# Kernel tuning notes

Measured on AMD Instinct MI355X. Metric: run time of the kernel, lower is better.

Reference implementation:

```python
import jax, jax.numpy as jnp
import numpy as np

HIDDEN = 768
INNER = 512
EPS = 1e-5


def setup_inputs() -> dict:
    key = jax.random.key(0)
    ks = jax.random.split(key, 6)
    B, S = 8, 4096
    x = jax.random.normal(ks[0], (B, S, HIDDEN), dtype=jnp.float32)
    W1 = jax.random.normal(ks[1], (INNER, HIDDEN), dtype=jnp.float32) * 0.02
    b1 = jnp.zeros((INNER,), dtype=jnp.float32)
    W2 = jax.random.normal(ks[2], (HIDDEN, INNER), dtype=jnp.float32) * 0.02
    b2 = jnp.zeros((HIDDEN,), dtype=jnp.float32)
    # output_proj: nn.Linear(hidden, hidden)
    bound = 1.0 / np.sqrt(HIDDEN)
    Wo = jax.random.uniform(ks[3], (HIDDEN, HIDDEN), minval=-bound, maxval=bound, dtype=jnp.float32)
    bo = jax.random.uniform(ks[4], (HIDDEN,), minval=-bound, maxval=bound, dtype=jnp.float32)
    # LayerNorm affine params
    gamma = jnp.ones((HIDDEN,), dtype=jnp.float32)
    beta = jnp.zeros((HIDDEN,), dtype=jnp.float32)
    return {"x": x, "W1": W1, "b1": b1, "W2": W2, "b2": b2,
            "Wo": Wo, "bo": bo, "gamma": gamma, "beta": beta}


def reference(x, W1, b1, W2, b2, Wo, bo, gamma, beta):
    # NOTE: the torch module's inner 'TTT update' loop never actually modifies
    # W1/b1/W2/b2 (loss computed, no step applied), so the math per token is
    # independent and fully vectorizable across (batch, seq).
    h = jax.nn.relu(jnp.einsum('bsd,id->bsi', x, W1) + b1)       # [B,S,INNER]
    pred = jnp.einsum('bsi,di->bsd', h, W2) + b2                 # [B,S,HIDDEN]
    out = jnp.einsum('bsd,ed->bse', pred, Wo) + bo               # output_proj
    # LayerNorm over last dim
    mu = jnp.mean(out, axis=-1, keepdims=True)
    var = jnp.mean(jnp.square(out - mu), axis=-1, keepdims=True)
    out = (out - mu) * jax.lax.rsqrt(var + EPS) * gamma + beta
    return out
```

## Files before the change

kernel.cpp:

```cpp
#include <hip/hip_runtime.h>
#include <hip/hip_bf16.h>


#define HIDDEN 768
#define INNER  512

typedef __bf16 bf16_t;
typedef bf16_t bf16x8 __attribute__((ext_vector_type(8)));
typedef bf16_t bf16x4 __attribute__((ext_vector_type(4)));
typedef float  f32x4  __attribute__((ext_vector_type(4)));

__device__ __forceinline__ void async16(const void* g, void* lds) {
  __builtin_amdgcn_global_load_lds(
      (const __attribute__((address_space(1))) unsigned int*)g,
      (__attribute__((address_space(3))) unsigned int*)lds, 16, 0, 0);
}

__global__ __launch_bounds__(256)
void prep(const float* __restrict__ x, const float* __restrict__ W1,
          const float* __restrict__ W2, const float* __restrict__ Wo,
          bf16_t* __restrict__ xb, bf16_t* __restrict__ W1b,
          bf16_t* __restrict__ W2t, bf16_t* __restrict__ Wob, int xb_blocks) {
  __shared__ float T[64][65];
  const int b = blockIdx.x, t = threadIdx.x;

  const float4* src; bf16x4* dst; int base;
  if (b < xb_blocks)            { src = (const float4*)x;  dst = (bf16x4*)xb;  base = b * 4096; }
  else if (b < xb_blocks + 24)  { src = (const float4*)W1; dst = (bf16x4*)W1b; base = (b - xb_blocks) * 4096; }
  else if (b < xb_blocks + 60)  { src = (const float4*)Wo; dst = (bf16x4*)Wob; base = (b - xb_blocks - 24) * 4096; }
  else {
    const int tile = b - xb_blocks - 60;
    const int d0 = (tile >> 3) << 6;
    const int i0 = (tile & 7) << 6;
#pragma unroll
    for (int j = 0; j < 4; ++j) {
      const int idx = j * 256 + t;
      const int r = idx >> 4, c4 = idx & 15;
      float4 v = *(const float4*)(W2 + (size_t)(d0 + r) * INNER + i0 + c4 * 4);
      T[r][c4 * 4 + 0] = v.x; T[r][c4 * 4 + 1] = v.y;
      T[r][c4 * 4 + 2] = v.z; T[r][c4 * 4 + 3] = v.w;
    }
    __syncthreads();
    const int i = t & 63, h4 = t >> 6;
    bf16x8 o0, o1;
#pragma unroll
    for (int c = 0; c < 8; ++c) { o0[c] = (bf16_t)T[h4 * 16 + c][i]; o1[c] = (bf16_t)T[h4 * 16 + 8 + c][i]; }
    bf16_t* orow = W2t + (size_t)(i0 + i) * HIDDEN + d0 + h4 * 16;
    *(bf16x8*)orow = o0;
    *(bf16x8*)(orow + 8) = o1;
    return;
  }
#pragma unroll
  for (int i = 0; i < 16; ++i) {
    float4 v = src[base + i * 256 + t];
    bf16x4 o;
    o[0] = (bf16_t)v.x; o[1] = (bf16_t)v.y; o[2] = (bf16_t)v.z; o[3] = (bf16_t)v.w;
    dst[base + i * 256 + t] = o;
  }
}

__global__ __launch_bounds__(256)
void beq_k(const float* __restrict__ Wo, const float* __restrict__ b2,
           const float* __restrict__ bo, float* __restrict__ beq) {
  const int e = blockIdx.x * 4 + (threadIdx.x >> 6);
  const int l = threadIdx.x & 63;
  float s = 0.f;
#pragma unroll
  for (int j = 0; j < 12; ++j) s += Wo[(size_t)e * HIDDEN + j * 64 + l] * b2[j * 64 + l];
#pragma unroll
  for (int off = 1; off < 64; off <<= 1) s += __shfl_xor(s, off, 64);
  if (l == 0) beq[e] = s + bo[e];
}

template <int N_, int K_, int MODE>
__global__ __launch_bounds__(256, 2)
void gemm_bt(const bf16_t* __restrict__ A, const bf16_t* __restrict__ Bt,
             const float* __restrict__ bias, bf16_t* __restrict__ Cout) {
  constexpr int NT = N_ / 128;
  constexpr int T  = K_ / 64;
  __shared__ __align__(16) bf16_t As[2][128 * 64];
  __shared__ __align__(16) bf16_t Bs[2][128 * 64];

  const int per = gridDim.x >> 3;
  const int nb  = (blockIdx.x & 7) * per + (blockIdx.x >> 3);
  const int m0 = (nb / NT) * 128;
  const int n0 = (nb % NT) * 128;

  const int tid = threadIdx.x;
  const int w = tid >> 6, l = tid & 63;
  const int wr = w >> 1, wc = w & 1;
  const int fr = l & 15, fq = l >> 4;

#define STAGE(dst, src, r0, k0)                                               \
  _Pragma("unroll") for (int i = 0; i < 4; ++i) {                             \
    const int G = i * 256 + tid, row = G >> 3, g = G & 7;                     \
    async16((src) + (size_t)((r0) + row) * K_ + (k0) + ((g ^ (row & 7)) << 3),\
            (char*)(dst) + (size_t)(i * 256 + w * 64) * 16);                  \
  }

  STAGE(As[0], A, m0, 0); STAGE(Bs[0], Bt, n0, 0);
  __syncthreads();

  f32x4 acc[4][4] = {};
#pragma unroll
  for (int t = 0; t < T; ++t) {
    const int cur = t & 1;
    if (t < T - 1) {
      STAGE(As[cur ^ 1], A, m0, (t + 1) * 64);
      STAGE(Bs[cur ^ 1], Bt, n0, (t + 1) * 64);
    }
#pragma unroll
    for (int kk = 0; kk < 2; ++kk) {
      bf16x8 ax[4], bx[4];
#pragma unroll
      for (int m = 0; m < 4; ++m) {
        const int row = wr * 64 + m * 16 + fr;
        const int slot = (kk * 4 + fq) ^ (row & 7);
        ax[m] = *(const bf16x8*)((const char*)As[cur] + row * 128 + slot * 16);
      }
#pragma unroll
      for (int n = 0; n < 4; ++n) {
        const int row = wc * 64 + n * 16 + fr;
        const int slot = (kk * 4 + fq) ^ (row & 7);
        bx[n] = *(const bf16x8*)((const char*)Bs[cur] + row * 128 + slot * 16);
      }
#pragma unroll
      for (int m = 0; m < 4; ++m)
#pragma unroll
        for (int n = 0; n < 4; ++n)
          acc[m][n] = __builtin_amdgcn_mfma_f32_16x16x32_bf16(ax[m], bx[n], acc[m][n], 0, 0, 0);
    }
    __syncthreads();
  }
#undef STAGE

  const int orow0 = m0 + wr * 64 + fq * 4;
  const int ocol0 = n0 + wc * 64 + fr;
#pragma unroll
  for (int n = 0; n < 4; ++n) {
    const int col = ocol0 + n * 16;
    const float bv = (MODE == 2) ? 0.f : bias[col];
#pragma unroll
    for (int m = 0; m < 4; ++m)
#pragma unroll
      for (int j = 0; j < 4; ++j) {
        float v = acc[m][n][j] + bv;
        if (MODE == 0) v = fmaxf(v, 0.f);
        Cout[(size_t)(orow0 + m * 16 + j) * N_ + col] = (bf16_t)v;
      }
  }
}

__global__ __launch_bounds__(256)
void ln_bf16(const bf16_t* __restrict__ raw, const float* __restrict__ gamma,
             const float* __restrict__ beta, float* __restrict__ out) {
  const int r = blockIdx.x * 4 + (threadIdx.x >> 6);
  const int l = threadIdx.x & 63;
  const bf16_t* rp = raw + (size_t)r * HIDDEN;
  float v[12];
  float s = 0.f, q = 0.f;
#pragma unroll
  for (int c = 0; c < 3; ++c) {
    bf16x4 b4 = *(const bf16x4*)(rp + c * 256 + l * 4);
#pragma unroll
    for (int j = 0; j < 4; ++j) {
      const float f = (float)b4[j];
      v[c * 4 + j] = f; s += f; q += f * f;
    }
  }
#pragma unroll
  for (int off = 1; off < 64; off <<= 1) {
    s += __shfl_xor(s, off, 64);
    q += __shfl_xor(q, off, 64);
  }
  const float mu  = s * (1.0f / HIDDEN);
  const float var = fmaxf(q * (1.0f / HIDDEN) - mu * mu, 0.f);
  const float inv = rsqrtf(var + 1e-5f);
  float* op = out + (size_t)r * HIDDEN;
#pragma unroll
  for (int c = 0; c < 3; ++c) {
    float4 g = ((const float4*)gamma)[c * 64 + l];
    float4 b = ((const float4*)beta)[c * 64 + l];
    float4 o;
    o.x = (v[c * 4 + 0] - mu) * inv * g.x + b.x;
    o.y = (v[c * 4 + 1] - mu) * inv * g.y + b.y;
    o.z = (v[c * 4 + 2] - mu) * inv * g.z + b.z;
    o.w = (v[c * 4 + 3] - mu) * inv * g.w + b.w;
    ((float4*)op)[c * 64 + l] = o;
  }
}

extern "C" void kernel_launch(void* const* d_in, const int* in_sizes, int n_in,
                              void* d_out, int out_size, void* d_ws, size_t ws_size,
                              hipStream_t stream) {
  const float* x     = (const float*)d_in[0];
  const float* W1    = (const float*)d_in[1];
  const float* b1    = (const float*)d_in[2];
  const float* W2    = (const float*)d_in[3];
  const float* b2    = (const float*)d_in[4];
  const float* Wo    = (const float*)d_in[5];
  const float* bo    = (const float*)d_in[6];
  const float* gamma = (const float*)d_in[7];
  const float* beta  = (const float*)d_in[8];

  const int M = in_sizes[0] / HIDDEN;

  char* ws = (char*)d_ws;
  bf16_t* xb   = (bf16_t*)ws;
  bf16_t* raw  = xb;
  bf16_t* h    = (bf16_t*)(ws + (size_t)M * HIDDEN * 2);
  bf16_t* W1b  = (bf16_t*)(ws + (size_t)M * HIDDEN * 2 + (size_t)M * INNER * 2);
  bf16_t* W2t  = W1b + INNER * HIDDEN;
  bf16_t* Wob  = W2t + INNER * HIDDEN;
  bf16_t* Weq  = Wob + HIDDEN * HIDDEN;
  float*  beq  = (float*)(Weq + HIDDEN * INNER);

  const int xb_blocks = (M * HIDDEN / 4) / 4096;

  prep<<<xb_blocks + 60 + 96, 256, 0, stream>>>(x, W1, W2, Wo, xb, W1b, W2t, Wob, xb_blocks);
  beq_k<<<HIDDEN / 4, 256, 0, stream>>>(Wo, b2, bo, beq);

  gemm_bt<INNER, HIDDEN, 2><<<(HIDDEN / 128) * (INNER / 128), 256, 0, stream>>>(Wob, W2t, nullptr, Weq);
  gemm_bt<INNER, HIDDEN, 0><<<(M / 128) * (INNER / 128), 256, 0, stream>>>(xb, W1b, b1, h);
  gemm_bt<HIDDEN, INNER, 1><<<(M / 128) * (HIDDEN / 128), 256, 0, stream>>>(h, Weq, beq, raw);
  ln_bf16<<<M / 4, 256, 0, stream>>>(raw, gamma, beta, (float*)d_out);
}
```

Measured before the change: 140.5 us.

## Use 128x256 tiles with triple-buffered async loads for the large GEMMs

The two large GEMMs move to a new kernel with 512-thread blocks and 128x256 output tiles. It uses a three-stage LDS ring filled by async global-to-LDS loads, explicit vmcnt waits so one stage stays in flight, and raised wave priority around the MFMA section. The aim is to hide global load latency and raise MFMA utilization through more B reuse per tile. The cost is a large LDS footprint (144 KB), which allows only one block per CU and halves the number of blocks in the grid. The small weight-folding GEMM is split into its own non-templated kernel with no bias.

```diff
diff --git a/kernel.cpp b/kernel.cpp
--- a/kernel.cpp
+++ b/kernel.cpp
@@ -72,12 +72,10 @@
   if (l == 0) beq[e] = s + bo[e];
 }
 
-template <int N_, int K_, int MODE>
 __global__ __launch_bounds__(256, 2)
-void gemm_bt(const bf16_t* __restrict__ A, const bf16_t* __restrict__ Bt,
-             const float* __restrict__ bias, bf16_t* __restrict__ Cout) {
-  constexpr int NT = N_ / 128;
-  constexpr int T  = K_ / 64;
+void gemm_small(const bf16_t* __restrict__ A, const bf16_t* __restrict__ Bt,
+                bf16_t* __restrict__ Cout) {
+  constexpr int N_ = INNER, K_ = HIDDEN, NT = N_ / 128, T = K_ / 64;
   __shared__ __align__(16) bf16_t As[2][128 * 64];
   __shared__ __align__(16) bf16_t Bs[2][128 * 64];
 
@@ -91,14 +89,14 @@
   const int wr = w >> 1, wc = w & 1;
   const int fr = l & 15, fq = l >> 4;
 
-#define STAGE(dst, src, r0, k0)                                               \
+#define STAGE2(dst, src, r0, k0)                                              \
   _Pragma("unroll") for (int i = 0; i < 4; ++i) {                             \
     const int G = i * 256 + tid, row = G >> 3, g = G & 7;                     \
     async16((src) + (size_t)((r0) + row) * K_ + (k0) + ((g ^ (row & 7)) << 3),\
             (char*)(dst) + (size_t)(i * 256 + w * 64) * 16);                  \
   }
 
-  STAGE(As[0], A, m0, 0); STAGE(Bs[0], Bt, n0, 0);
+  STAGE2(As[0], A, m0, 0); STAGE2(Bs[0], Bt, n0, 0);
   __syncthreads();
 
   f32x4 acc[4][4] = {};
@@ -106,8 +104,8 @@
   for (int t = 0; t < T; ++t) {
     const int cur = t & 1;
     if (t < T - 1) {
-      STAGE(As[cur ^ 1], A, m0, (t + 1) * 64);
-      STAGE(Bs[cur ^ 1], Bt, n0, (t + 1) * 64);
+      STAGE2(As[cur ^ 1], A, m0, (t + 1) * 64);
+      STAGE2(Bs[cur ^ 1], Bt, n0, (t + 1) * 64);
     }
 #pragma unroll
     for (int kk = 0; kk < 2; ++kk) {
@@ -132,14 +130,103 @@
     }
     __syncthreads();
   }
-#undef STAGE
+#undef STAGE2
 
   const int orow0 = m0 + wr * 64 + fq * 4;
   const int ocol0 = n0 + wc * 64 + fr;
 #pragma unroll
+  for (int n = 0; n < 4; ++n)
+#pragma unroll
+    for (int m = 0; m < 4; ++m)
+#pragma unroll
+      for (int j = 0; j < 4; ++j)
+        Cout[(size_t)(orow0 + m * 16 + j) * N_ + ocol0 + n * 16] = (bf16_t)acc[m][n][j];
+}
+
+template <int N_, int K_, int MODE>
+__global__ __launch_bounds__(512, 1)
+void gemm_p3(const bf16_t* __restrict__ A, const bf16_t* __restrict__ Bt,
+             const float* __restrict__ bias, bf16_t* __restrict__ Cout) {
+  constexpr int NT = N_ / 256;
+  constexpr int T  = K_ / 64;
+  __shared__ __align__(16) bf16_t As[3][128 * 64];
+  __shared__ __align__(16) bf16_t Bs[3][256 * 64];
+
+  const int per = gridDim.x >> 3;
+  const int nb  = (blockIdx.x & 7) * per + (blockIdx.x >> 3);
+  const int m0 = (nb / NT) * 128;
+  const int n0 = (nb % NT) * 256;
+
+  const int tid = threadIdx.x;
+  const int w = tid >> 6, l = tid & 63;
+  const int wm = w >> 2, wn = w & 3;
+  const int fr = l & 15, fq = l >> 4;
+
+#define STAGE_A(buf, k0)                                                      \
+  _Pragma("unroll") for (int i = 0; i < 2; ++i) {                             \
+    const int G = i * 512 + tid, row = G >> 3, g = G & 7;                     \
+    async16(A + (size_t)(m0 + row) * K_ + (k0) + ((g ^ (row & 7)) << 3),      \
+            (char*)As[buf] + (size_t)(i * 512 + w * 64) * 16);                \
+  }
+#define STAGE_B(buf, k0)                                                      \
+  _Pragma("unroll") for (int i = 0; i < 4; ++i) {                             \
+    const int G = i * 512 + tid, row = G >> 3, g = G & 7;                     \
+    async16(Bt + (size_t)(n0 + row) * K_ + (k0) + ((g ^ (row & 7)) << 3),     \
+            (char*)Bs[buf] + (size_t)(i * 512 + w * 64) * 16);                \
+  }
+
+  STAGE_A(0, 0);  STAGE_B(0, 0);
+  STAGE_A(1, 64); STAGE_B(1, 64);
+  asm volatile("s_waitcnt vmcnt(6)" ::: "memory");
+  __builtin_amdgcn_s_barrier();
+
+  f32x4 acc[4][4] = {};
+#pragma unroll
+  for (int t = 0; t < T; ++t) {
+    const int cur = t % 3;
+    if (t + 2 < T) {
+      const int nx = (t + 2) % 3;
+      STAGE_A(nx, (t + 2) * 64);
+      STAGE_B(nx, (t + 2) * 64);
+    }
+    __builtin_amdgcn_s_setprio(1);
+#pragma unroll
+    for (int kk = 0; kk < 2; ++kk) {
+      bf16x8 ax[4], bx[4];
+#pragma unroll
+      for (int m = 0; m < 4; ++m) {
+        const int row = wm * 64 + m * 16 + fr;
+        const int slot = (kk * 4 + fq) ^ (row & 7);
+        ax[m] = *(const bf16x8*)((const char*)As[cur] + row * 128 + slot * 16);
+      }
+#pragma unroll
+      for (int n = 0; n < 4; ++n) {
+        const int row = wn * 64 + n * 16 + fr;
+        const int slot = (kk * 4 + fq) ^ (row & 7);
+        bx[n] = *(const bf16x8*)((const char*)Bs[cur] + row * 128 + slot * 16);
+      }
+#pragma unroll
+      for (int m = 0; m < 4; ++m)
+#pragma unroll
+        for (int n = 0; n < 4; ++n)
+          acc[m][n] = __builtin_amdgcn_mfma_f32_16x16x32_bf16(ax[m], bx[n], acc[m][n], 0, 0, 0);
+    }
+    __builtin_amdgcn_s_setprio(0);
+    if (t < T - 1) {
+      if (t + 2 < T) asm volatile("s_waitcnt vmcnt(6)" ::: "memory");
+      else           asm volatile("s_waitcnt vmcnt(0)" ::: "memory");
+      __builtin_amdgcn_s_barrier();
+    }
+  }
+#undef STAGE_A
+#undef STAGE_B
+
+  const int orow0 = m0 + wm * 64 + fq * 4;
+  const int ocol0 = n0 + wn * 64 + fr;
+#pragma unroll
   for (int n = 0; n < 4; ++n) {
     const int col = ocol0 + n * 16;
-    const float bv = (MODE == 2) ? 0.f : bias[col];
+    const float bv = bias[col];
 #pragma unroll
     for (int m = 0; m < 4; ++m)
 #pragma unroll
@@ -220,8 +307,8 @@
   prep<<<xb_blocks + 60 + 96, 256, 0, stream>>>(x, W1, W2, Wo, xb, W1b, W2t, Wob, xb_blocks);
   beq_k<<<HIDDEN / 4, 256, 0, stream>>>(Wo, b2, bo, beq);
 
-  gemm_bt<INNER, HIDDEN, 2><<<(HIDDEN / 128) * (INNER / 128), 256, 0, stream>>>(Wob, W2t, nullptr, Weq);
-  gemm_bt<INNER, HIDDEN, 0><<<(M / 128) * (INNER / 128), 256, 0, stream>>>(xb, W1b, b1, h);
-  gemm_bt<HIDDEN, INNER, 1><<<(M / 128) * (HIDDEN / 128), 256, 0, stream>>>(h, Weq, beq, raw);
+  gemm_small<<<(HIDDEN / 128) * (INNER / 128), 256, 0, stream>>>(Wob, W2t, Weq);
+  gemm_p3<INNER, HIDDEN, 0><<<(M / 128) * (INNER / 256), 512, 0, stream>>>(xb, W1b, b1, h);
+  gemm_p3<HIDDEN, INNER, 1><<<(M / 128) * (HIDDEN / 256), 512, 0, stream>>>(h, Weq, beq, raw);
   ln_bf16<<<M / 4, 256, 0, stream>>>(raw, gamma, beta, (float*)d_out);
 }
```

Result: slower. 144.7 us (+3.0%).

## Fuse x conversion, both token GEMMs and LayerNorm into one megakernel

Applied to the files above, without the earlier changes.

Replaces the x-to-bf16 prep pass, the two token GEMMs and the separate LayerNorm kernel with one kernel per 64-row tile. It loads fp32 x directly into LDS and converts it in registers. The ReLU hidden activations stay in LDS instead of going through global memory, and LayerNorm is computed from the accumulators using LDS atomics. This removes the global round trips for xb, h and raw, but uses about 152KB of LDS at one block per CU with 512 threads, so occupancy and latency hiding are limited.

```diff
diff --git a/kernel.cpp b/kernel.cpp
--- a/kernel.cpp
+++ b/kernel.cpp
@@ -17,19 +17,17 @@
 }
 
 __global__ __launch_bounds__(256)
-void prep(const float* __restrict__ x, const float* __restrict__ W1,
-          const float* __restrict__ W2, const float* __restrict__ Wo,
-          bf16_t* __restrict__ xb, bf16_t* __restrict__ W1b,
-          bf16_t* __restrict__ W2t, bf16_t* __restrict__ Wob, int xb_blocks) {
+void prep(const float* __restrict__ W1, const float* __restrict__ W2,
+          const float* __restrict__ Wo, bf16_t* __restrict__ W1b,
+          bf16_t* __restrict__ W2t, bf16_t* __restrict__ Wob) {
   __shared__ float T[64][65];
   const int b = blockIdx.x, t = threadIdx.x;
 
   const float4* src; bf16x4* dst; int base;
-  if (b < xb_blocks)            { src = (const float4*)x;  dst = (bf16x4*)xb;  base = b * 4096; }
-  else if (b < xb_blocks + 24)  { src = (const float4*)W1; dst = (bf16x4*)W1b; base = (b - xb_blocks) * 4096; }
-  else if (b < xb_blocks + 60)  { src = (const float4*)Wo; dst = (bf16x4*)Wob; base = (b - xb_blocks - 24) * 4096; }
+  if (b < 24)       { src = (const float4*)W1; dst = (bf16x4*)W1b; base = b * 4096; }
+  else if (b < 60)  { src = (const float4*)Wo; dst = (bf16x4*)Wob; base = (b - 24) * 4096; }
   else {
-    const int tile = b - xb_blocks - 60;
+    const int tile = b - 60;
     const int d0 = (tile >> 3) << 6;
     const int i0 = (tile & 7) << 6;
 #pragma unroll
@@ -72,17 +70,14 @@
   if (l == 0) beq[e] = s + bo[e];
 }
 
-template <int N_, int K_, int MODE>
 __global__ __launch_bounds__(256, 2)
-void gemm_bt(const bf16_t* __restrict__ A, const bf16_t* __restrict__ Bt,
-             const float* __restrict__ bias, bf16_t* __restrict__ Cout) {
-  constexpr int NT = N_ / 128;
-  constexpr int T  = K_ / 64;
+void gemm_weq(const bf16_t* __restrict__ A, const bf16_t* __restrict__ Bt,
+              bf16_t* __restrict__ Cout) {
+  constexpr int N_ = INNER, K_ = HIDDEN, NT = N_ / 128, T = K_ / 64;
   __shared__ __align__(16) bf16_t As[2][128 * 64];
   __shared__ __align__(16) bf16_t Bs[2][128 * 64];
 
-  const int per = gridDim.x >> 3;
-  const int nb  = (blockIdx.x & 7) * per + (blockIdx.x >> 3);
+  const int nb = blockIdx.x;
   const int m0 = (nb / NT) * 128;
   const int n0 = (nb % NT) * 128;
 
@@ -91,14 +86,14 @@
   const int wr = w >> 1, wc = w & 1;
   const int fr = l & 15, fq = l >> 4;
 
-#define STAGE(dst, src, r0, k0)                                               \
+#define STAGEW(dst, src, r0, k0)                                              \
   _Pragma("unroll") for (int i = 0; i < 4; ++i) {                             \
     const int G = i * 256 + tid, row = G >> 3, g = G & 7;                     \
     async16((src) + (size_t)((r0) + row) * K_ + (k0) + ((g ^ (row & 7)) << 3),\
             (char*)(dst) + (size_t)(i * 256 + w * 64) * 16);                  \
   }
 
-  STAGE(As[0], A, m0, 0); STAGE(Bs[0], Bt, n0, 0);
+  STAGEW(As[0], A, m0, 0); STAGEW(Bs[0], Bt, n0, 0);
   __syncthreads();
 
   f32x4 acc[4][4] = {};
@@ -106,8 +101,8 @@
   for (int t = 0; t < T; ++t) {
     const int cur = t & 1;
     if (t < T - 1) {
-      STAGE(As[cur ^ 1], A, m0, (t + 1) * 64);
-      STAGE(Bs[cur ^ 1], Bt, n0, (t + 1) * 64);
+      STAGEW(As[cur ^ 1], A, m0, (t + 1) * 64);
+      STAGEW(Bs[cur ^ 1], Bt, n0, (t + 1) * 64);
     }
 #pragma unroll
     for (int kk = 0; kk < 2; ++kk) {
@@ -132,62 +127,194 @@
     }
     __syncthreads();
   }
-#undef STAGE
+#undef STAGEW
 
   const int orow0 = m0 + wr * 64 + fq * 4;
   const int ocol0 = n0 + wc * 64 + fr;
 #pragma unroll
-  for (int n = 0; n < 4; ++n) {
-    const int col = ocol0 + n * 16;
-    const float bv = (MODE == 2) ? 0.f : bias[col];
+  for (int n = 0; n < 4; ++n)
 #pragma unroll
     for (int m = 0; m < 4; ++m)
 #pragma unroll
+      for (int j = 0; j < 4; ++j)
+        Cout[(size_t)(orow0 + m * 16 + j) * N_ + ocol0 + n * 16] = (bf16_t)acc[m][n][j];
+}
+
+__global__ __launch_bounds__(512, 1)
+void mega(const float* __restrict__ x, const bf16_t* __restrict__ W1b,
+          const float* __restrict__ b1, const bf16_t* __restrict__ Weq,
+          const float* __restrict__ beq, const float* __restrict__ gamma,
+          const float* __restrict__ beta, float* __restrict__ out) {
+  __shared__ __align__(16) char L[155648];
+  char* hS = L;
+  char* A1 = L + 65536;
+  char* B1 = L + 65536 + 24576;
+  char* B2 = L + 65536;
+  float* sn = (float*)L;
+
+  const int tid = threadIdx.x;
+  const int w = tid >> 6, l = tid & 63;
+  const int wm = w >> 2, wn = w & 3;
+  const int fr = l & 15, fq = l >> 4;
+  const int gm0 = blockIdx.x * 64;
+
+#define STAGE_A1(buf, k0) {                                                   \
+    const int row = tid >> 3, g = tid & 7;                                    \
+    async16(x + (size_t)(gm0 + row) * HIDDEN + (k0) + ((g ^ (row & 7)) << 2), \
+            A1 + (buf) * 8192 + tid * 16);                                    \
+  }
+#define STAGE_B1(buf, k0)                                                     \
+  _Pragma("unroll") for (int i = 0; i < 4; ++i) {                             \
+    const int G = i * 512 + tid, row = G >> 2, g = G & 3;                     \
+    const int sl = g ^ (row & 3) ^ ((row & 4) >> 1);                          \
+    async16(W1b + (size_t)row * HIDDEN + (k0) + (sl << 3),                    \
+            B1 + (buf) * 32768 + G * 16);                                     \
+  }
+
+  STAGE_B1(0, 0);
+  STAGE_A1(0, 0);
+  STAGE_A1(1, 32);
+  asm volatile("s_waitcnt vmcnt(1)" ::: "memory");
+  __builtin_amdgcn_s_barrier();
+
+  f32x4 acc1[2][8] = {};
+#pragma unroll 6
+  for (int t = 0; t < 24; ++t) {
+    if (t + 1 < 24) STAGE_B1((t + 1) & 1, (t + 1) * 32);
+    if (t + 2 < 24) STAGE_A1((t + 2) % 3, (t + 2) * 32);
+    const char* Ab = A1 + (t % 3) * 8192;
+    const char* Bb = B1 + (t & 1) * 32768;
+    __builtin_amdgcn_s_setprio(1);
+    bf16x8 ax[2];
+#pragma unroll
+    for (int m = 0; m < 2; ++m) {
+      const int row = wm * 32 + m * 16 + fr;
+      const int p0 = (2 * fq) ^ (row & 7), p1 = (2 * fq + 1) ^ (row & 7);
+      f32x4 q0 = *(const f32x4*)(Ab + row * 128 + p0 * 16);
+      f32x4 q1 = *(const f32x4*)(Ab + row * 128 + p1 * 16);
+      bf16x8 a;
+#pragma unroll
+      for (int c = 0; c < 4; ++c) { a[c] = (bf16_t)q0[c]; a[4 + c] = (bf16_t)q1[c]; }
+      ax[m] = a;
+    }
+#pragma unroll
+    for (int n = 0; n < 8; ++n) {
+      const int row = wn * 128 + n * 16 + fr;
+      const int sl = fq ^ (row & 3) ^ ((row & 4) >> 1);
+      bf16x8 bx = *(const bf16x8*)(Bb + row * 64 + sl * 16);
+#pragma unroll
+      for (int m = 0; m < 2; ++m)
+        acc1[m][n] = __builtin_amdgcn_mfma_f32_16x16x32_bf16(ax[m], bx, acc1[m][n], 0, 0, 0);
+    }
+    __builtin_amdgcn_s_setprio(0);
+    if (t < 23) {
+      if (t + 2 < 24) asm volatile("s_waitcnt vmcnt(1)" ::: "memory");
+      else            asm volatile("s_waitcnt vmcnt(0)" ::: "memory");
+      __builtin_amdgcn_s_barrier();
+    }
+  }
+#undef STAGE_A1
+#undef STAGE_B1
+
+#pragma unroll
+  for (int n = 0; n < 8; ++n) {
+    const int col = wn * 128 + n * 16 + fr;
+    const float bv = b1[col];
+    const int g0 = col >> 3, b2c = (col & 7) * 2;
+#pragma unroll
+    for (int m = 0; m < 2; ++m)
+#pragma unroll
       for (int j = 0; j < 4; ++j) {
-        float v = acc[m][n][j] + bv;
-        if (MODE == 0) v = fmaxf(v, 0.f);
-        Cout[(size_t)(orow0 + m * 16 + j) * N_ + col] = (bf16_t)v;
-      }
-  }
-}
-
-__global__ __launch_bounds__(256)
-void ln_bf16(const bf16_t* __restrict__ raw, const float* __restrict__ gamma,
-             const float* __restrict__ beta, float* __restrict__ out) {
-  const int r = blockIdx.x * 4 + (threadIdx.x >> 6);
-  const int l = threadIdx.x & 63;
-  const bf16_t* rp = raw + (size_t)r * HIDDEN;
-  float v[12];
-  float s = 0.f, q = 0.f;
-#pragma unroll
-  for (int c = 0; c < 3; ++c) {
-    bf16x4 b4 = *(const bf16x4*)(rp + c * 256 + l * 4);
+        const int row = wm * 32 + m * 16 + fq * 4 + j;
+        *(bf16_t*)(hS + row * 1024 + (g0 ^ (row & 7)) * 16 + b2c) =
+            (bf16_t)fmaxf(acc1[m][n][j] + bv, 0.f);
+      }
+  }
+  __syncthreads();
+
+  f32x4 acc2[2][12] = {};
+#pragma unroll 2
+  for (int t = 0; t < 16; ++t) {
+#pragma unroll
+    for (int i = 0; i < 6; ++i) {
+      const int G = i * 512 + tid, row = G >> 2, g = G & 3;
+      const int sl = g ^ (row & 3) ^ ((row & 4) >> 1);
+      async16(Weq + (size_t)row * INNER + t * 32 + (sl << 3), B2 + G * 16);
+    }
+    __syncthreads();
+    __builtin_amdgcn_s_setprio(1);
+    bf16x8 ax[2];
+#pragma unroll
+    for (int m = 0; m < 2; ++m) {
+      const int row = wm * 32 + m * 16 + fr;
+      const int g = t * 4 + fq;
+      ax[m] = *(const bf16x8*)(hS + row * 1024 + (g ^ (row & 7)) * 16);
+    }
+#pragma unroll
+    for (int n = 0; n < 12; ++n) {
+      const int row = wn * 192 + n * 16 + fr;
+      const int sl = fq ^ (row & 3) ^ ((row & 4) >> 1);
+      bf16x8 bx = *(const bf16x8*)(B2 + row * 64 + sl * 16);
+#pragma unroll
+      for (int m = 0; m < 2; ++m)
+        acc2[m][n] = __builtin_amdgcn_mfma_f32_16x16x32_bf16(ax[m], bx, acc2[m][n], 0, 0, 0);
+    }
+    __builtin_amdgcn_s_setprio(0);
+    __syncthreads();
+  }
+
+  if (tid < 128) sn[tid] = 0.f;
+  __syncthreads();
+#pragma unroll
+  for (int n = 0; n < 12; ++n) {
+    const float bv = beq[wn * 192 + n * 16 + fr];
+#pragma unroll
+    for (int m = 0; m < 2; ++m)
+#pragma unroll
+      for (int j = 0; j < 4; ++j) acc2[m][n][j] += bv;
+  }
+#pragma unroll
+  for (int m = 0; m < 2; ++m)
 #pragma unroll
     for (int j = 0; j < 4; ++j) {
-      const float f = (float)b4[j];
-      v[c * 4 + j] = f; s += f; q += f * f;
-    }
-  }
-#pragma unroll
-  for (int off = 1; off < 64; off <<= 1) {
-    s += __shfl_xor(s, off, 64);
-    q += __shfl_xor(q, off, 64);
-  }
-  const float mu  = s * (1.0f / HIDDEN);
-  const float var = fmaxf(q * (1.0f / HIDDEN) - mu * mu, 0.f);
-  const float inv = rsqrtf(var + 1e-5f);
-  float* op = out + (size_t)r * HIDDEN;
-#pragma unroll
-  for (int c = 0; c < 3; ++c) {
-    float4 g = ((const float4*)gamma)[c * 64 + l];
-    float4 b = ((const float4*)beta)[c * 64 + l];
-    float4 o;
-    o.x = (v[c * 4 + 0] - mu) * inv * g.x + b.x;
-    o.y = (v[c * 4 + 1] - mu) * inv * g.y + b.y;
-    o.z = (v[c * 4 + 2] - mu) * inv * g.z + b.z;
-    o.w = (v[c * 4 + 3] - mu) * inv * g.w + b.w;
-    ((float4*)op)[c * 64 + l] = o;
-  }
+      float s = 0.f, q = 0.f;
+#pragma unroll
+      for (int n = 0; n < 12; ++n) {
+        const float v = acc2[m][n][j];
+        s += v; q += v * v;
+      }
+#pragma unroll
+      for (int off = 1; off < 16; off <<= 1) {
+        s += __shfl_xor(s, off, 64);
+        q += __shfl_xor(q, off, 64);
+      }
+      if (fr == 0) {
+        const int row = wm * 32 + m * 16 + fq * 4 + j;
+        atomicAdd(&sn[row], s);
+        atomicAdd(&sn[64 + row], q);
+      }
+    }
+  __syncthreads();
+
+  float gv[12], bw[12];
+#pragma unroll
+  for (int n = 0; n < 12; ++n) {
+    const int col = wn * 192 + n * 16 + fr;
+    gv[n] = gamma[col]; bw[n] = beta[col];
+  }
+#pragma unroll
+  for (int m = 0; m < 2; ++m)
+#pragma unroll
+    for (int j = 0; j < 4; ++j) {
+      const int row = wm * 32 + m * 16 + fq * 4 + j;
+      const float mu  = sn[row] * (1.0f / HIDDEN);
+      const float var = fmaxf(sn[64 + row] * (1.0f / HIDDEN) - mu * mu, 0.f);
+      const float inv = rsqrtf(var + 1e-5f);
+      float* orow = out + (size_t)(gm0 + row) * HIDDEN;
+#pragma unroll
+      for (int n = 0; n < 12; ++n)
+        orow[wn * 192 + n * 16 + fr] = (acc2[m][n][j] - mu) * inv * gv[n] + bw[n];
+    }
 }
 
 extern "C" void kernel_launch(void* const* d_in, const int* in_sizes, int n_in,
@@ -206,22 +333,14 @@
   const int M = in_sizes[0] / HIDDEN;
 
   char* ws = (char*)d_ws;
-  bf16_t* xb   = (bf16_t*)ws;
-  bf16_t* raw  = xb;
-  bf16_t* h    = (bf16_t*)(ws + (size_t)M * HIDDEN * 2);
-  bf16_t* W1b  = (bf16_t*)(ws + (size_t)M * HIDDEN * 2 + (size_t)M * INNER * 2);
-  bf16_t* W2t  = W1b + INNER * HIDDEN;
-  bf16_t* Wob  = W2t + INNER * HIDDEN;
-  bf16_t* Weq  = Wob + HIDDEN * HIDDEN;
-  float*  beq  = (float*)(Weq + HIDDEN * INNER);
-
-  const int xb_blocks = (M * HIDDEN / 4) / 4096;
-
-  prep<<<xb_blocks + 60 + 96, 256, 0, stream>>>(x, W1, W2, Wo, xb, W1b, W2t, Wob, xb_blocks);
+  bf16_t* W1b = (bf16_t*)ws;
+  bf16_t* W2t = W1b + INNER * HIDDEN;
+  bf16_t* Wob = W2t + INNER * HIDDEN;
+  bf16_t* Weq = Wob + HIDDEN * HIDDEN;
+  float*  beq = (float*)(Weq + HIDDEN * INNER);
+
+  prep<<<156, 256, 0, stream>>>(W1, W2, Wo, W1b, W2t, Wob);
   beq_k<<<HIDDEN / 4, 256, 0, stream>>>(Wo, b2, bo, beq);
-
-  gemm_bt<INNER, HIDDEN, 2><<<(HIDDEN / 128) * (INNER / 128), 256, 0, stream>>>(Wob, W2t, nullptr, Weq);
-  gemm_bt<INNER, HIDDEN, 0><<<(M / 128) * (INNER / 128), 256, 0, stream>>>(xb, W1b, b1, h);
-  gemm_bt<HIDDEN, INNER, 1><<<(M / 128) * (HIDDEN / 128), 256, 0, stream>>>(h, Weq, beq, raw);
-  ln_bf16<<<M / 4, 256, 0, stream>>>(raw, gamma, beta, (float*)d_out);
-}
+  gemm_weq<<<(HIDDEN / 128) * (INNER / 128), 256, 0, stream>>>(Wob, W2t, Weq);
+  mega<<<M / 64, 512, 0, stream>>>(x, W1b, b1, Weq, beq, gamma, beta, (float*)d_out);
+}
```

After: 134.6 us. 4.2% less time.

## Fold bias kernel into prep, split Weq GEMM, use vmcnt waits in main GEMM

Applied to the files above, without the earlier changes.

The bias-folding reduction moves into extra blocks of the prep kernel, which removes one launch. The small Weq GEMM becomes its own non-templated kernel. In the main GEMMs, the full __syncthreads after each tile load is replaced by an explicit s_waitcnt vmcnt(8) plus a raw s_barrier, so the next tile's async loads stay in flight while the current tile is computed. The partial vmcnt wait depends on the exact count of outstanding global_load_lds ops (8 per stage) and on the compiler not reordering them, so a wrong count could cause races.

```diff
diff --git a/kernel.cpp b/kernel.cpp
--- a/kernel.cpp
+++ b/kernel.cpp
@@ -19,16 +19,18 @@
 __global__ __launch_bounds__(256)
 void prep(const float* __restrict__ x, const float* __restrict__ W1,
           const float* __restrict__ W2, const float* __restrict__ Wo,
+          const float* __restrict__ b2, const float* __restrict__ bo,
           bf16_t* __restrict__ xb, bf16_t* __restrict__ W1b,
-          bf16_t* __restrict__ W2t, bf16_t* __restrict__ Wob, int xb_blocks) {
+          bf16_t* __restrict__ W2t, bf16_t* __restrict__ Wob,
+          float* __restrict__ beq, int xb_blocks) {
   __shared__ float T[64][65];
   const int b = blockIdx.x, t = threadIdx.x;
 
   const float4* src; bf16x4* dst; int base;
-  if (b < xb_blocks)            { src = (const float4*)x;  dst = (bf16x4*)xb;  base = b * 4096; }
-  else if (b < xb_blocks + 24)  { src = (const float4*)W1; dst = (bf16x4*)W1b; base = (b - xb_blocks) * 4096; }
-  else if (b < xb_blocks + 60)  { src = (const float4*)Wo; dst = (bf16x4*)Wob; base = (b - xb_blocks - 24) * 4096; }
-  else {
+  if (b < xb_blocks)           { src = (const float4*)x;  dst = (bf16x4*)xb;  base = b * 4096; }
+  else if (b < xb_blocks + 24) { src = (const float4*)W1; dst = (bf16x4*)W1b; base = (b - xb_blocks) * 4096; }
+  else if (b < xb_blocks + 60) { src = (const float4*)Wo; dst = (bf16x4*)Wob; base = (b - xb_blocks - 24) * 4096; }
+  else if (b < xb_blocks + 156) {
     const int tile = b - xb_blocks - 60;
     const int d0 = (tile >> 3) << 6;
     const int i0 = (tile & 7) << 6;
@@ -49,6 +51,16 @@
     *(bf16x8*)orow = o0;
     *(bf16x8*)(orow + 8) = o1;
     return;
+  } else {
+    const int e = (b - xb_blocks - 156) * 4 + (t >> 6);
+    const int l = t & 63;
+    float s = 0.f;
+#pragma unroll
+    for (int j = 0; j < 12; ++j) s += Wo[(size_t)e * HIDDEN + j * 64 + l] * b2[j * 64 + l];
+#pragma unroll
+    for (int off = 1; off < 64; off <<= 1) s += __shfl_xor(s, off, 64);
+    if (l == 0) beq[e] = s + bo[e];
+    return;
   }
 #pragma unroll
   for (int i = 0; i < 16; ++i) {
@@ -59,17 +71,74 @@
   }
 }
 
-__global__ __launch_bounds__(256)
-void beq_k(const float* __restrict__ Wo, const float* __restrict__ b2,
-           const float* __restrict__ bo, float* __restrict__ beq) {
-  const int e = blockIdx.x * 4 + (threadIdx.x >> 6);
-  const int l = threadIdx.x & 63;
-  float s = 0.f;
-#pragma unroll
-  for (int j = 0; j < 12; ++j) s += Wo[(size_t)e * HIDDEN + j * 64 + l] * b2[j * 64 + l];
-#pragma unroll
-  for (int off = 1; off < 64; off <<= 1) s += __shfl_xor(s, off, 64);
-  if (l == 0) beq[e] = s + bo[e];
+__global__ __launch_bounds__(256, 2)
+void gemm_weq(const bf16_t* __restrict__ A, const bf16_t* __restrict__ Bt,
+              bf16_t* __restrict__ Cout) {
+  constexpr int N_ = INNER, K_ = HIDDEN, NT = N_ / 128, T = K_ / 64;
+  __shared__ __align__(16) bf16_t As[2][128 * 64];
+  __shared__ __align__(16) bf16_t Bs[2][128 * 64];
+
+  const int nb = blockIdx.x;
+  const int m0 = (nb / NT) * 128;
+  const int n0 = (nb % NT) * 128;
+
+  const int tid = threadIdx.x;
+  const int w = tid >> 6, l = tid & 63;
+  const int wr = w >> 1, wc = w & 1;
+  const int fr = l & 15, fq = l >> 4;
+
+#define STAGEW(dst, src, r0, k0)                                              \
+  _Pragma("unroll") for (int i = 0; i < 4; ++i) {                             \
+    const int G = i * 256 + tid, row = G >> 3, g = G & 7;                     \
+    async16((src) + (size_t)((r0) + row) * K_ + (k0) + ((g ^ (row & 7)) << 3),\
+            (char*)(dst) + (size_t)(i * 256 + w * 64) * 16);                  \
+  }
+
+  STAGEW(As[0], A, m0, 0); STAGEW(Bs[0], Bt, n0, 0);
+  __syncthreads();
+
+  f32x4 acc[4][4] = {};
+#pragma unroll
+  for (int t = 0; t < T; ++t) {
+    const int cur = t & 1;
+    if (t < T - 1) {
+      STAGEW(As[cur ^ 1], A, m0, (t + 1) * 64);
+      STAGEW(Bs[cur ^ 1], Bt, n0, (t + 1) * 64);
+    }
+#pragma unroll
+    for (int kk = 0; kk < 2; ++kk) {
+      bf16x8 ax[4], bx[4];
+#pragma unroll
+      for (int m = 0; m < 4; ++m) {
+        const int row = wr * 64 + m * 16 + fr;
+        const int slot = (kk * 4 + fq) ^ (row & 7);
+        ax[m] = *(const bf16x8*)((const char*)As[cur] + row * 128 + slot * 16);
+      }
+#pragma unroll
+      for (int n = 0; n < 4; ++n) {
+        const int row = wc * 64 + n * 16 + fr;
+        const int slot = (kk * 4 + fq) ^ (row & 7);
+        bx[n] = *(const bf16x8*)((const char*)Bs[cur] + row * 128 + slot * 16);
+      }
+#pragma unroll
+      for (int m = 0; m < 4; ++m)
+#pragma unroll
+        for (int n = 0; n < 4; ++n)
+          acc[m][n] = __builtin_amdgcn_mfma_f32_16x16x32_bf16(ax[m], bx[n], acc[m][n], 0, 0, 0);
+    }
+    __syncthreads();
+  }
+#undef STAGEW
+
+  const int orow0 = m0 + wr * 64 + fq * 4;
+  const int ocol0 = n0 + wc * 64 + fr;
+#pragma unroll
+  for (int n = 0; n < 4; ++n)
+#pragma unroll
+    for (int m = 0; m < 4; ++m)
+#pragma unroll
+      for (int j = 0; j < 4; ++j)
+        Cout[(size_t)(orow0 + m * 16 + j) * N_ + ocol0 + n * 16] = (bf16_t)acc[m][n][j];
 }
 
 template <int N_, int K_, int MODE>
@@ -99,16 +168,19 @@
   }
 
   STAGE(As[0], A, m0, 0); STAGE(Bs[0], Bt, n0, 0);
-  __syncthreads();
 
   f32x4 acc[4][4] = {};
 #pragma unroll
   for (int t = 0; t < T; ++t) {
     const int cur = t & 1;
-    if (t < T - 1) {
+    if (t + 1 < T) {
       STAGE(As[cur ^ 1], A, m0, (t + 1) * 64);
       STAGE(Bs[cur ^ 1], Bt, n0, (t + 1) * 64);
-    }
+      asm volatile("s_waitcnt vmcnt(8)" ::: "memory");
+    } else {
+      asm volatile("s_waitcnt vmcnt(0)" ::: "memory");
+    }
+    __builtin_amdgcn_s_barrier();
 #pragma unroll
     for (int kk = 0; kk < 2; ++kk) {
       bf16x8 ax[4], bx[4];
@@ -130,7 +202,7 @@
         for (int n = 0; n < 4; ++n)
           acc[m][n] = __builtin_amdgcn_mfma_f32_16x16x32_bf16(ax[m], bx[n], acc[m][n], 0, 0, 0);
     }
-    __syncthreads();
+    __builtin_amdgcn_s_barrier();
   }
 #undef STAGE
 
@@ -139,7 +211,7 @@
 #pragma unroll
   for (int n = 0; n < 4; ++n) {
     const int col = ocol0 + n * 16;
-    const float bv = (MODE == 2) ? 0.f : bias[col];
+    const float bv = bias[col];
 #pragma unroll
     for (int m = 0; m < 4; ++m)
 #pragma unroll
@@ -217,10 +289,9 @@
 
   const int xb_blocks = (M * HIDDEN / 4) / 4096;
 
-  prep<<<xb_blocks + 60 + 96, 256, 0, stream>>>(x, W1, W2, Wo, xb, W1b, W2t, Wob, xb_blocks);
-  beq_k<<<HIDDEN / 4, 256, 0, stream>>>(Wo, b2, bo, beq);
-
-  gemm_bt<INNER, HIDDEN, 2><<<(HIDDEN / 128) * (INNER / 128), 256, 0, stream>>>(Wob, W2t, nullptr, Weq);
+  prep<<<xb_blocks + 156 + 192, 256, 0, stream>>>(x, W1, W2, Wo, b2, bo,
+                                                  xb, W1b, W2t, Wob, beq, xb_blocks);
+  gemm_weq<<<(HIDDEN / 128) * (INNER / 128), 256, 0, stream>>>(Wob, W2t, Weq);
   gemm_bt<INNER, HIDDEN, 0><<<(M / 128) * (INNER / 128), 256, 0, stream>>>(xb, W1b, b1, h);
   gemm_bt<HIDDEN, INNER, 1><<<(M / 128) * (HIDDEN / 128), 256, 0, stream>>>(h, Weq, beq, raw);
   ln_bf16<<<M / 4, 256, 0, stream>>>(raw, gamma, beta, (float*)d_out);
```

Result: faster. 133.0 us (-5.3%).
